# Optimization experiments

Measured on AMD Instinct MI355X. Metric: run time of the kernel, lower is better.

Reference implementation:

```python
import jax, jax.numpy as jnp
import numpy as np


def setup_inputs() -> dict:
    key = jax.random.key(0)
    k1, k2 = jax.random.split(key)
    preds = jax.random.normal(k1, (16, 19, 512, 512), dtype=jnp.float32)
    targets = jax.random.randint(k2, (16, 1024, 1024), 0, 19, dtype=jnp.int64)
    return {"preds": preds, "targets": targets, "grid_size": 16}


def reference(preds, targets, grid_size):
    # preds: (B, nc, H, W) logits; targets: (B, Ht, Wt) int labels in [0, nc)
    B, nc, H, W = preds.shape
    Ht, Wt = targets.shape[1], targets.shape[2]
    g = grid_size

    # _scale_target: nearest-neighbor resize of label map to preds spatial size
    rows = (jnp.arange(H) * Ht) // H
    cols = (jnp.arange(W) * Wt) // W
    t = targets[:, rows][:, :, cols]  # (B, H, W)

    # _get_batch_label_vector: grid-wise class-presence histogram
    Hc, Wc = H // g, W // g  # H, W chosen divisible by g (pad branch is no-op)
    cells = t.reshape(B, Hc, g, Wc, g).transpose(0, 1, 3, 2, 4)
    cells = cells.reshape(B * Hc * Wc, g * g)  # (N, g*g) labels per grid cell
    N = B * Hc * Wc
    # scatter-count per cell (fused on-device replacement of per-sample histc loop)
    counts = jnp.zeros((N, nc), preds.dtype).at[jnp.arange(N)[:, None], cells].add(1.0)
    presence = (counts > 0).astype(preds.dtype)  # (N, nc) multi-label vector

    # broadcast each cell's presence vector back to its pixels -> (B, nc, H, W)
    se = presence.reshape(B, Hc, Wc, nc)
    se = jnp.repeat(jnp.repeat(se, g, axis=1), g, axis=2)  # (B, H, W, nc)
    se = se.transpose(0, 3, 1, 2)

    # BCE(sigmoid(preds), se), reduction='mean' (numerically stable form)
    logp = jax.nn.log_sigmoid(preds)
    log1mp = jax.nn.log_sigmoid(-preds)
    return jnp.mean(-(se * logp + (1.0 - se) * log1mp))
```

## Files before the change

kernel.cpp:

```cpp
#include <hip/hip_runtime.h>
#include <cstdint>


#define B_   16
#define NC_  19
#define H_   512
#define W_   512
#define G_   16
#define HC_  32
#define WC_  32
#define NCELL (B_ * HC_ * WC_)
#define W4_  (W_ / 4)
#define TOTAL4 (B_ * NC_ * H_ * W4_)
#define INV_TOTAL (1.0f / (float)((long long)B_ * NC_ * H_ * W_))

__global__ __launch_bounds__(256) void presence_kernel(
    const int* __restrict__ targets,
    uint32_t* __restrict__ masks,
    float* __restrict__ out)
{
    const int cell = blockIdx.x;
    const int tid  = threadIdx.x;

    if (cell == 0 && tid == 0) out[0] = 0.0f;

    const int cj = cell & 31;
    const int ci = (cell >> 5) & 31;
    const int b  = cell >> 10;

    const int u = tid >> 4;
    const int v = tid & 15;
    const int row = 2 * (ci * G_ + u);
    const int col = 2 * (cj * G_ + v);

    const int lab = targets[((b << 10) + row) * 1024 + col];
    unsigned m = 1u << lab;

    #pragma unroll
    for (int off = 32; off >= 1; off >>= 1)
        m |= __shfl_xor(m, off, 64);

    __shared__ unsigned s_mask;
    if (tid == 0) s_mask = 0u;
    __syncthreads();
    if ((tid & 63) == 0) atomicOr(&s_mask, m);
    __syncthreads();
    if (tid == 0) masks[cell] = s_mask;
}

__global__ __launch_bounds__(256) void bce_kernel(
    const float* __restrict__ preds,
    const uint32_t* __restrict__ masks,
    float* __restrict__ out)
{
    const int tid    = threadIdx.x;
    const int gidx   = blockIdx.x * blockDim.x + tid;
    const int stride = gridDim.x * blockDim.x;

    float acc = 0.0f;

    for (int i4 = gidx; i4 < TOTAL4; i4 += stride) {
        const int j4  = i4 & (W4_ - 1);
        const int t1  = i4 >> 7;
        const int row = t1 & (H_ - 1);
        const int t2  = t1 >> 9;
        const int c   = t2 % NC_;
        const int b   = t2 / NC_;

        const uint32_t m = masks[(b << 10) + ((row >> 4) << 5) + (j4 >> 2)];
        const float se = (float)((m >> c) & 1u);

        const float4 x = ((const float4*)preds)[i4];

        float a, t;
        a = fabsf(x.x); t = __logf(1.0f + __expf(-a));
        acc += fmaxf(x.x, 0.0f) - se * x.x + t;
        a = fabsf(x.y); t = __logf(1.0f + __expf(-a));
        acc += fmaxf(x.y, 0.0f) - se * x.y + t;
        a = fabsf(x.z); t = __logf(1.0f + __expf(-a));
        acc += fmaxf(x.z, 0.0f) - se * x.z + t;
        a = fabsf(x.w); t = __logf(1.0f + __expf(-a));
        acc += fmaxf(x.w, 0.0f) - se * x.w + t;
    }

    #pragma unroll
    for (int off = 32; off >= 1; off >>= 1)
        acc += __shfl_down(acc, off, 64);

    __shared__ float s_part[4];
    const int wave = tid >> 6;
    if ((tid & 63) == 0) s_part[wave] = acc;
    __syncthreads();

    if (tid == 0) {
        float s = s_part[0] + s_part[1] + s_part[2] + s_part[3];
        atomicAdd(out, s * INV_TOTAL);
    }
}

extern "C" void kernel_launch(void* const* d_in, const int* in_sizes, int n_in,
                              void* d_out, int out_size, void* d_ws, size_t ws_size,
                              hipStream_t stream)
{
    const float* preds   = (const float*)d_in[0];
    const int*   targets = (const int*)d_in[1];

    uint32_t* masks = (uint32_t*)d_ws;
    float*    out   = (float*)d_out;

    presence_kernel<<<NCELL, 256, 0, stream>>>(targets, masks, out);

    const int blocks = 4096;
    bce_kernel<<<blocks, 256, 0, stream>>>(preds, masks, out);
}
```

Baseline: 465.2 us.

## Fuse presence mask computation into BCE kernel per grid-cell row

Merges the presence-mask kernel and the BCE reduction into one kernel where each block handles one row of grid cells for one batch. The block builds the 32 cell masks in shared memory from the targets, then streams all 19 channels for its 16 image rows. This drops the global mask buffer and its round trip, and removes the per-element index division. The grid shrinks to 512 blocks of 512 threads with fixed per-thread work, which may reduce latency hiding and balance on a large GPU. A separate tiny kernel now zeroes the output.

Result: no change. 457.1 us (-1.7%).

```diff
diff --git a/kernel.cpp b/kernel.cpp
--- a/kernel.cpp
+++ b/kernel.cpp
@@ -9,91 +9,84 @@
 #define G_   16
 #define HC_  32
 #define WC_  32
-#define NCELL (B_ * HC_ * WC_)
 #define W4_  (W_ / 4)
-#define TOTAL4 (B_ * NC_ * H_ * W4_)
+#define CSTRIDE4 (H_ * W4_)
 #define INV_TOTAL (1.0f / (float)((long long)B_ * NC_ * H_ * W_))
 
-__global__ __launch_bounds__(256) void presence_kernel(
+__global__ __launch_bounds__(64) void zero_kernel(float* __restrict__ out)
+{
+    if (threadIdx.x == 0) out[0] = 0.0f;
+}
+
+__device__ __forceinline__ float bce4(const float4 x, const float se)
+{
+    float r;
+    r  = fmaxf(x.x, 0.0f) - se * x.x + __logf(1.0f + __expf(-fabsf(x.x)));
+    r += fmaxf(x.y, 0.0f) - se * x.y + __logf(1.0f + __expf(-fabsf(x.y)));
+    r += fmaxf(x.z, 0.0f) - se * x.z + __logf(1.0f + __expf(-fabsf(x.z)));
+    r += fmaxf(x.w, 0.0f) - se * x.w + __logf(1.0f + __expf(-fabsf(x.w)));
+    return r;
+}
+
+__global__ __launch_bounds__(512) void fused_kernel(
+    const float* __restrict__ preds,
     const int* __restrict__ targets,
-    uint32_t* __restrict__ masks,
     float* __restrict__ out)
 {
-    const int cell = blockIdx.x;
-    const int tid  = threadIdx.x;
+    const int blk = blockIdx.x;
+    const int tid = threadIdx.x;
+    const int ci  = blk & (HC_ - 1);
+    const int b   = blk >> 5;
 
-    if (cell == 0 && tid == 0) out[0] = 0.0f;
+    __shared__ unsigned s_mask[WC_];
+    if (tid < WC_) s_mask[tid] = 0u;
+    __syncthreads();
 
-    const int cj = cell & 31;
-    const int ci = (cell >> 5) & 31;
-    const int b  = cell >> 10;
+    {
+        const int cj  = tid >> 4;
+        const int v   = tid & 15;
+        const int col = ((cj << 4) + v) << 1;
+        const int trow0 = (b << 10) + (ci << 5);
+        unsigned m = 0u;
+        #pragma unroll
+        for (int u = 0; u < 16; ++u)
+            m |= 1u << targets[((trow0 + (u << 1)) << 10) + col];
+        atomicOr(&s_mask[cj], m);
+    }
+    __syncthreads();
 
-    const int u = tid >> 4;
-    const int v = tid & 15;
-    const int row = 2 * (ci * G_ + u);
-    const int col = 2 * (cj * G_ + v);
+    const int j4 = tid & (W4_ - 1);
+    const int r0 = tid >> 7;
+    const unsigned mword = s_mask[j4 >> 2];
 
-    const int lab = targets[((b << 10) + row) * 1024 + col];
-    unsigned m = 1u << lab;
-
-    #pragma unroll
-    for (int off = 32; off >= 1; off >>= 1)
-        m |= __shfl_xor(m, off, 64);
-
-    __shared__ unsigned s_mask;
-    if (tid == 0) s_mask = 0u;
-    __syncthreads();
-    if ((tid & 63) == 0) atomicOr(&s_mask, m);
-    __syncthreads();
-    if (tid == 0) masks[cell] = s_mask;
-}
-
-__global__ __launch_bounds__(256) void bce_kernel(
-    const float* __restrict__ preds,
-    const uint32_t* __restrict__ masks,
-    float* __restrict__ out)
-{
-    const int tid    = threadIdx.x;
-    const int gidx   = blockIdx.x * blockDim.x + tid;
-    const int stride = gridDim.x * blockDim.x;
+    const float4* pb = (const float4*)preds
+        + (size_t)b * NC_ * CSTRIDE4
+        + (size_t)(ci * G_ + r0) * W4_ + j4;
 
     float acc = 0.0f;
-
-    for (int i4 = gidx; i4 < TOTAL4; i4 += stride) {
-        const int j4  = i4 & (W4_ - 1);
-        const int t1  = i4 >> 7;
-        const int row = t1 & (H_ - 1);
-        const int t2  = t1 >> 9;
-        const int c   = t2 % NC_;
-        const int b   = t2 / NC_;
-
-        const uint32_t m = masks[(b << 10) + ((row >> 4) << 5) + (j4 >> 2)];
-        const float se = (float)((m >> c) & 1u);
-
-        const float4 x = ((const float4*)preds)[i4];
-
-        float a, t;
-        a = fabsf(x.x); t = __logf(1.0f + __expf(-a));
-        acc += fmaxf(x.x, 0.0f) - se * x.x + t;
-        a = fabsf(x.y); t = __logf(1.0f + __expf(-a));
-        acc += fmaxf(x.y, 0.0f) - se * x.y + t;
-        a = fabsf(x.z); t = __logf(1.0f + __expf(-a));
-        acc += fmaxf(x.z, 0.0f) - se * x.z + t;
-        a = fabsf(x.w); t = __logf(1.0f + __expf(-a));
-        acc += fmaxf(x.w, 0.0f) - se * x.w + t;
+    for (int c = 0; c < NC_; ++c) {
+        const float se = (float)((mword >> c) & 1u);
+        const float4 x0 = pb[(size_t)c * CSTRIDE4];
+        const float4 x1 = pb[(size_t)c * CSTRIDE4 +  4 * W4_];
+        const float4 x2 = pb[(size_t)c * CSTRIDE4 +  8 * W4_];
+        const float4 x3 = pb[(size_t)c * CSTRIDE4 + 12 * W4_];
+        acc += bce4(x0, se);
+        acc += bce4(x1, se);
+        acc += bce4(x2, se);
+        acc += bce4(x3, se);
     }
 
     #pragma unroll
     for (int off = 32; off >= 1; off >>= 1)
         acc += __shfl_down(acc, off, 64);
 
-    __shared__ float s_part[4];
-    const int wave = tid >> 6;
-    if ((tid & 63) == 0) s_part[wave] = acc;
+    __shared__ float s_part[8];
+    if ((tid & 63) == 0) s_part[tid >> 6] = acc;
     __syncthreads();
-
     if (tid == 0) {
-        float s = s_part[0] + s_part[1] + s_part[2] + s_part[3];
+        float s = 0.0f;
+        #pragma unroll
+        for (int w = 0; w < 8; ++w) s += s_part[w];
         atomicAdd(out, s * INV_TOTAL);
     }
 }
@@ -104,12 +97,8 @@
 {
     const float* preds   = (const float*)d_in[0];
     const int*   targets = (const int*)d_in[1];
+    float* out = (float*)d_out;
 
-    uint32_t* masks = (uint32_t*)d_ws;
-    float*    out   = (float*)d_out;
-
-    presence_kernel<<<NCELL, 256, 0, stream>>>(targets, masks, out);
-
-    const int blocks = 4096;
-    bce_kernel<<<blocks, 256, 0, stream>>>(preds, masks, out);
+    zero_kernel<<<1, 64, 0, stream>>>(out);
+    fused_kernel<<<B_ * HC_, 512, 0, stream>>>(preds, targets, out);
 }
```
